# Kernel optimization log

Measured on AMD Instinct MI355X. Metric: run time of the kernel, lower is better.

Reference implementation:

```python
import jax, jax.numpy as jnp
import numpy as np

N = 768
C_IN = 128
C_OUT = 64
C_DGRAM = 39
C_AA = 22
C_ESM = 1280
LN_EPS = 1e-5


def _layer_norm(x, g, b):
    mu = jnp.mean(x, axis=-1, keepdims=True)
    var = jnp.var(x, axis=-1, keepdims=True)
    return (x - mu) * jax.lax.rsqrt(var + LN_EPS) * g + b


def setup_inputs() -> dict:
    key = jax.random.key(0)
    ks = jax.random.split(key, 36)
    rn = lambda k, s, sc=1.0: jax.random.normal(k, s, dtype=jnp.float32) * sc
    ru = lambda k, s: jax.random.uniform(k, s, dtype=jnp.float32)
    w = lambda k, cin: rn(k, (cin, C_OUT), 1.0 / np.sqrt(cin))
    z = jnp.zeros((C_OUT,), jnp.float32)
    return {
        "template_dgram": rn(ks[0], (N, N, C_DGRAM)),
        "aatype_one_hot": ru(ks[1], (N, C_AA)),
        "query_embedding": rn(ks[2], (N, N, C_IN)),
        "pseudo_beta_mask": ru(ks[3], (N,)),
        "backbone_mask": ru(ks[4], (N,)),
        "multichain_mask_2d": ru(ks[5], (N, N)),
        "unit_x": rn(ks[6], (N, N)),
        "unit_y": rn(ks[7], (N, N)),
        "unit_z": rn(ks[8], (N, N)),
        "esm_embedding": rn(ks[9], (N, C_ESM)),
        "w_dgram": w(ks[10], C_DGRAM), "b_dgram": z,
        "w_aa1": w(ks[11], C_AA), "b_aa1": z,
        "w_aa2": w(ks[12], C_AA), "b_aa2": z,
        "ln_g": jnp.ones((C_IN,), jnp.float32), "ln_b": jnp.zeros((C_IN,), jnp.float32),
        "w_q": w(ks[13], C_IN), "b_q": z,
        "w_pbm": w(ks[14], 1), "b_pbm": z,
        "w_x": w(ks[15], 1), "b_x": z,
        "w_y": w(ks[16], 1), "b_y": z,
        "w_z": w(ks[17], 1), "b_z": z,
        "w_bb": w(ks[18], 1), "b_bb": z,
        "w_esm1": w(ks[19], C_ESM), "b_esm1": z,
        "w_esm2": w(ks[20], C_ESM), "b_esm2": z,
    }


def reference(template_dgram, aatype_one_hot, query_embedding, pseudo_beta_mask,
              backbone_mask, multichain_mask_2d, unit_x, unit_y, unit_z, esm_embedding,
              w_dgram, b_dgram, w_aa1, b_aa1, w_aa2, b_aa2, ln_g, ln_b, w_q, b_q,
              w_pbm, b_pbm, w_x, b_x, w_y, b_y, w_z, b_z, w_bb, b_bb,
              w_esm1, b_esm1, w_esm2, b_esm2):
    # pair masks [N, N]
    pb2 = pseudo_beta_mask[:, None] * pseudo_beta_mask[None, :] * multichain_mask_2d
    bb2 = backbone_mask[:, None] * backbone_mask[None, :] * multichain_mask_2d
    # masked distogram -> GEMM over bins
    act = jnp.einsum('ijd,do->ijo', template_dgram * bb2[..., None], w_dgram) + b_dgram
    # Linear(1, c_out) branches: scalar * weight row + bias (broadcasts)
    act = act + (pb2[..., None] * w_pbm[0] + b_pbm)
    # per-residue aatype projections broadcast over rows / columns
    act = act + (aatype_one_hot @ w_aa1 + b_aa1)[None, :, :]
    act = act + (aatype_one_hot @ w_aa2 + b_aa2)[:, None, :]
    act = act + ((unit_x * bb2)[..., None] * w_x[0] + b_x)
    act = act + ((unit_y * bb2)[..., None] * w_y[0] + b_y)
    act = act + ((unit_z * bb2)[..., None] * w_z[0] + b_z)
    act = act + (bb2[..., None] * w_bb[0] + b_bb)
    # per-residue ESM projections broadcast over rows / columns
    act = act + (esm_embedding @ w_esm1 + b_esm1)[None, :, :]
    act = act + (esm_embedding @ w_esm2 + b_esm2)[:, None, :]
    # LayerNorm + projection of the query pair embedding [N, N, c_in]
    q = _layer_norm(query_embedding, ln_g, ln_b)
    act = act + jnp.einsum('ijc,co->ijo', q, w_q) + b_q
    return act
```

## Files before the change

### kernel.cpp

```cpp
#include <hip/hip_runtime.h>

#define NN 768
#define CIN 128
#define COUT 64
#define CDG 39
#define CAA 22
#define CESM 1280

typedef __attribute__((ext_vector_type(8))) short short8;
typedef __attribute__((ext_vector_type(4))) float f32x4;

__device__ __forceinline__ unsigned short f2bf(float f) {
  union { float f; unsigned int i; } c; c.f = f;
  unsigned int u = c.i;
  u += 0x7fffu + ((u >> 16) & 1u);
  return (unsigned short)(u >> 16);
}
__device__ __forceinline__ unsigned int pk(float a, float b) {
  return (unsigned int)f2bf(a) | ((unsigned int)f2bf(b) << 16);
}

struct Args {
  const float *td, *aa, *q, *pbm, *bbm, *mc, *ux, *uy, *uz, *esm;
  const float *w_dgram, *b_dgram, *w_aa1, *b_aa1, *w_aa2, *b_aa2;
  const float *ln_g, *ln_b, *w_q, *b_q;
  const float *w_pbm, *b_pbm, *w_x, *b_x, *w_y, *b_y, *w_z, *b_z, *w_bb, *b_bb;
  const float *w_esm1, *b_esm1, *w_esm2, *b_esm2;
  float* out;
  float* row_vec; float* col_vec; unsigned short* b_pack;
};

__global__ __launch_bounds__(256) void k_pre(Args a) {
  const int b = blockIdx.x;
  const int tid = threadIdx.x;
  if (b == NN) {
    for (int e = tid; e < 12288; e += 256) {
      int jj = e & 7;
      int lane = (e >> 3) & 63;
      int qt = e >> 9;
      int q = qt >> 2, t = qt & 3;
      int k = q * 32 + ((lane >> 4) << 3) + jj;
      int n = t * 16 + (lane & 15);
      float v = 0.f;
      if (k < CIN) v = a.w_q[k * COUT + n];
      else if (k < CIN + CDG) v = a.w_dgram[(k - CIN) * COUT + n];
      else if (k == 167) v = a.w_pbm[n];
      else if (k == 168) v = a.w_x[n];
      else if (k == 169) v = a.w_y[n];
      else if (k == 170) v = a.w_z[n];
      else if (k == 171) v = a.w_bb[n];
      a.b_pack[e] = f2bf(v);
    }
    return;
  }
  const int wv = tid >> 6, lane = tid & 63;
  float acc1 = 0.f, acc2 = 0.f;
  const int KT = CAA + CESM;
  const int SL = (KT + 3) / 4;
  int k0 = wv * SL;
  int k1 = k0 + SL; if (k1 > KT) k1 = KT;
  for (int k = k0; k < k1; ++k) {
    float v; const float *w1, *w2;
    if (k < CAA) { v = a.aa[b * CAA + k]; w1 = a.w_aa1 + k * COUT; w2 = a.w_aa2 + k * COUT; }
    else { int e = k - CAA; v = a.esm[b * CESM + e]; w1 = a.w_esm1 + e * COUT; w2 = a.w_esm2 + e * COUT; }
    acc1 += v * w1[lane];
    acc2 += v * w2[lane];
  }
  __shared__ float red1[4][64];
  __shared__ float red2[4][64];
  red1[wv][lane] = acc1; red2[wv][lane] = acc2;
  __syncthreads();
  if (wv == 0) {
    float r1 = red1[0][lane] + red1[1][lane] + red1[2][lane] + red1[3][lane];
    float r2 = red2[0][lane] + red2[1][lane] + red2[2][lane] + red2[3][lane];
    float br = a.b_aa1[lane] + a.b_esm1[lane] + a.b_dgram[lane] +
               a.b_pbm[lane] + a.b_x[lane] + a.b_y[lane] +
               a.b_z[lane] + a.b_bb[lane] + a.b_q[lane];
    float bc = a.b_aa2[lane] + a.b_esm2[lane];
    a.row_vec[b * COUT + lane] = r1 + br;
    a.col_vec[b * COUT + lane] = r2 + bc;
  }
}

__global__ __launch_bounds__(256, 3) void k_main(Args a) {
  const int jt = blockIdx.x;
  const int i  = blockIdx.y;
  const int jbase = jt * 64;
  const int tid = threadIdx.x;
  const int wv = tid >> 6, lane = tid & 63;

  __shared__ unsigned short A_lds[64][200];
  __shared__ unsigned short B_lds[12288];
  __shared__ float bb2_s[64];
  __shared__ float pb2_s[64];

  if (tid < 64) {
    int j = jbase + tid;
    float mc  = a.mc[(size_t)i * NN + j];
    bb2_s[tid] = a.bbm[i] * a.bbm[j] * mc;
    pb2_s[tid] = a.pbm[i] * a.pbm[j] * mc;
  }

  {
    const int4* src = (const int4*)a.b_pack;
    int4* dst = (int4*)B_lds;
#pragma unroll
    for (int r = 0; r < 6; ++r) dst[tid + 256 * r] = src[tid + 256 * r];
  }

  {
    const int p = tid >> 2, s = tid & 3;
    const float* qrow = a.q + ((size_t)i * NN + jbase + p) * CIN + s * 32;
    float q32[32];
    const float4* qv = (const float4*)qrow;
#pragma unroll
    for (int blk = 0; blk < 8; ++blk) {
      float4 t4 = qv[blk];
      q32[blk * 4 + 0] = t4.x; q32[blk * 4 + 1] = t4.y;
      q32[blk * 4 + 2] = t4.z; q32[blk * 4 + 3] = t4.w;
    }
    float sum = 0.f, sq = 0.f;
#pragma unroll
    for (int c = 0; c < 32; ++c) { sum += q32[c]; sq += q32[c] * q32[c]; }
    sum += __shfl_xor(sum, 1); sum += __shfl_xor(sum, 2);
    sq  += __shfl_xor(sq, 1);  sq  += __shfl_xor(sq, 2);
    float mu  = sum * (1.f / 128.f);
    float var = sq * (1.f / 128.f) - mu * mu;
    float rs  = rsqrtf(var + 1e-5f);
    float gl[32], bl[32];
    const float4* gv = (const float4*)(a.ln_g + s * 32);
    const float4* hv = (const float4*)(a.ln_b + s * 32);
#pragma unroll
    for (int blk = 0; blk < 8; ++blk) {
      float4 g4 = gv[blk], h4 = hv[blk];
      gl[blk * 4 + 0] = g4.x; gl[blk * 4 + 1] = g4.y;
      gl[blk * 4 + 2] = g4.z; gl[blk * 4 + 3] = g4.w;
      bl[blk * 4 + 0] = h4.x; bl[blk * 4 + 1] = h4.y;
      bl[blk * 4 + 2] = h4.z; bl[blk * 4 + 3] = h4.w;
    }
    int4* dA = (int4*)&A_lds[p][s * 32];
#pragma unroll
    for (int blk = 0; blk < 4; ++blk) {
      union { int4 v; unsigned int w[4]; } o;
#pragma unroll
      for (int w2 = 0; w2 < 4; ++w2) {
        int c = blk * 8 + w2 * 2;
        o.w[w2] = pk((q32[c] - mu) * rs * gl[c] + bl[c],
                     (q32[c + 1] - mu) * rs * gl[c + 1] + bl[c + 1]);
      }
      dA[blk] = o.v;
    }
  }
  __syncthreads();

  {
    const float* base = a.td + ((size_t)i * NN + jbase) * CDG;
    const float2* src = (const float2*)base;
    for (int w = tid; w < (64 * CDG) / 2; w += 256) {
      float2 d2 = src[w];
      int f0 = w * 2;
      int p0 = (f0 * 26887) >> 20; int d0 = f0 - p0 * CDG;
      int f1 = f0 + 1;
      int p1 = (f1 * 26887) >> 20; int d1 = f1 - p1 * CDG;
      A_lds[p0][CIN + d0] = f2bf(d2.x * bb2_s[p0]);
      A_lds[p1][CIN + d1] = f2bf(d2.y * bb2_s[p1]);
    }
  }
  if (tid < 64) {
    int p = tid;
    size_t gij = (size_t)i * NN + jbase + p;
    float bb = bb2_s[p];
    A_lds[p][167] = f2bf(pb2_s[p]);
    A_lds[p][168] = f2bf(a.ux[gij] * bb);
    A_lds[p][169] = f2bf(a.uy[gij] * bb);
    A_lds[p][170] = f2bf(a.uz[gij] * bb);
    A_lds[p][171] = f2bf(bb);
    unsigned int* zp = (unsigned int*)&A_lds[p][172];
#pragma unroll
    for (int z = 0; z < 10; ++z) zp[z] = 0;
  }
  __syncthreads();

  f32x4 acc[4];
#pragma unroll
  for (int t = 0; t < 4; ++t) { f32x4 z = {0.f, 0.f, 0.f, 0.f}; acc[t] = z; }
  const int m = lane & 15, quad = lane >> 4;
  const unsigned short* Ab = &A_lds[wv * 16 + m][quad * 8];
  const unsigned short* Bb = &B_lds[lane * 8];
#pragma unroll
  for (int q = 0; q < 6; ++q) {
    short8 af = *(const short8*)(Ab + q * 32);
#pragma unroll
    for (int t = 0; t < 4; ++t) {
      short8 bfr = *(const short8*)(Bb + (q * 4 + t) * 512);
      acc[t] = __builtin_amdgcn_mfma_f32_16x16x32_bf16(af, bfr, acc[t], 0, 0, 0);
    }
  }

  const float* cvp = a.col_vec + (size_t)i * COUT;
#pragma unroll
  for (int t = 0; t < 4; ++t) {
    int n = t * 16 + m;
    float cv = cvp[n];
#pragma unroll
    for (int r = 0; r < 4; ++r) {
      int p = wv * 16 + quad * 4 + r;
      int j = jbase + p;
      float val = acc[t][r] + a.row_vec[j * COUT + n] + cv;
      a.out[((size_t)i * NN + j) * COUT + n] = val;
    }
  }
}

extern "C" void kernel_launch(void* const* d_in, const int* in_sizes, int n_in,
                              void* d_out, int out_size, void* d_ws, size_t ws_size,
                              hipStream_t stream) {
  Args a;
  a.td     = (const float*)d_in[0];
  a.aa     = (const float*)d_in[1];
  a.q      = (const float*)d_in[2];
  a.pbm    = (const float*)d_in[3];
  a.bbm    = (const float*)d_in[4];
  a.mc     = (const float*)d_in[5];
  a.ux     = (const float*)d_in[6];
  a.uy     = (const float*)d_in[7];
  a.uz     = (const float*)d_in[8];
  a.esm    = (const float*)d_in[9];
  a.w_dgram = (const float*)d_in[10]; a.b_dgram = (const float*)d_in[11];
  a.w_aa1   = (const float*)d_in[12]; a.b_aa1   = (const float*)d_in[13];
  a.w_aa2   = (const float*)d_in[14]; a.b_aa2   = (const float*)d_in[15];
  a.ln_g    = (const float*)d_in[16]; a.ln_b    = (const float*)d_in[17];
  a.w_q     = (const float*)d_in[18]; a.b_q     = (const float*)d_in[19];
  a.w_pbm   = (const float*)d_in[20]; a.b_pbm   = (const float*)d_in[21];
  a.w_x     = (const float*)d_in[22]; a.b_x     = (const float*)d_in[23];
  a.w_y     = (const float*)d_in[24]; a.b_y     = (const float*)d_in[25];
  a.w_z     = (const float*)d_in[26]; a.b_z     = (const float*)d_in[27];
  a.w_bb    = (const float*)d_in[28]; a.b_bb    = (const float*)d_in[29];
  a.w_esm1  = (const float*)d_in[30]; a.b_esm1  = (const float*)d_in[31];
  a.w_esm2  = (const float*)d_in[32]; a.b_esm2  = (const float*)d_in[33];
  a.out = (float*)d_out;
  a.row_vec = (float*)d_ws;
  a.col_vec = a.row_vec + NN * COUT;
  a.b_pack  = (unsigned short*)(a.col_vec + NN * COUT);

  hipLaunchKernelGGL(k_pre, dim3(NN + 1), dim3(256), 0, stream, a);
  hipLaunchKernelGGL(k_main, dim3(12, NN), dim3(256), 0, stream, a);
}
```

Baseline: 803.5 us.

## Load query rows directly into MFMA fragments and fold LayerNorm affine into weights

Each lane now loads its query-embedding slice straight into registers in the MFMA A-fragment layout, computes the LayerNorm statistics with cross-lane shuffles, and packs bf16 fragments without staging them through LDS. The LayerNorm gain is folded into the packed w_q weights and the LayerNorm bias projection into the row bias vector in the pre-kernel. This shrinks the LDS A tile to the distogram and scalar part only and raises the occupancy hint from 3 to 4 blocks. The aim is to cut LDS traffic, LDS footprint and per-element arithmetic, at the cost of more live registers per thread.

```diff
diff --git a/kernel.cpp b/kernel.cpp
--- a/kernel.cpp
+++ b/kernel.cpp
@@ -42,7 +42,7 @@
       int k = q * 32 + ((lane >> 4) << 3) + jj;
       int n = t * 16 + (lane & 15);
       float v = 0.f;
-      if (k < CIN) v = a.w_q[k * COUT + n];
+      if (k < CIN) v = a.ln_g[k] * a.w_q[k * COUT + n];
       else if (k < CIN + CDG) v = a.w_dgram[(k - CIN) * COUT + n];
       else if (k == 167) v = a.w_pbm[n];
       else if (k == 168) v = a.w_x[n];
@@ -73,26 +73,37 @@
   if (wv == 0) {
     float r1 = red1[0][lane] + red1[1][lane] + red1[2][lane] + red1[3][lane];
     float r2 = red2[0][lane] + red2[1][lane] + red2[2][lane] + red2[3][lane];
+    float bq = 0.f;
+    for (int c = 0; c < CIN; ++c) bq += a.ln_b[c] * a.w_q[c * COUT + lane];
     float br = a.b_aa1[lane] + a.b_esm1[lane] + a.b_dgram[lane] +
                a.b_pbm[lane] + a.b_x[lane] + a.b_y[lane] +
-               a.b_z[lane] + a.b_bb[lane] + a.b_q[lane];
+               a.b_z[lane] + a.b_bb[lane] + a.b_q[lane] + bq;
     float bc = a.b_aa2[lane] + a.b_esm2[lane];
     a.row_vec[b * COUT + lane] = r1 + br;
     a.col_vec[b * COUT + lane] = r2 + bc;
   }
 }
 
-__global__ __launch_bounds__(256, 3) void k_main(Args a) {
+__global__ __launch_bounds__(256, 4) void k_main(Args a) {
   const int jt = blockIdx.x;
   const int i  = blockIdx.y;
   const int jbase = jt * 64;
   const int tid = threadIdx.x;
   const int wv = tid >> 6, lane = tid & 63;
-
-  __shared__ unsigned short A_lds[64][200];
+  const int m = lane & 15, quad = lane >> 4;
+
   __shared__ unsigned short B_lds[12288];
+  __shared__ unsigned short A2[64][72];
   __shared__ float bb2_s[64];
   __shared__ float pb2_s[64];
+
+  const float* qrow = a.q + ((size_t)i * NN + jbase + wv * 16 + m) * CIN + quad * 8;
+  float4 qv[8];
+#pragma unroll
+  for (int qq = 0; qq < 4; ++qq) {
+    qv[2 * qq]     = *(const float4*)(qrow + qq * 32);
+    qv[2 * qq + 1] = *(const float4*)(qrow + qq * 32 + 4);
+  }
 
   if (tid < 64) {
     int j = jbase + tid;
@@ -108,49 +119,31 @@
     for (int r = 0; r < 6; ++r) dst[tid + 256 * r] = src[tid + 256 * r];
   }
 
-  {
-    const int p = tid >> 2, s = tid & 3;
-    const float* qrow = a.q + ((size_t)i * NN + jbase + p) * CIN + s * 32;
-    float q32[32];
-    const float4* qv = (const float4*)qrow;
-#pragma unroll
-    for (int blk = 0; blk < 8; ++blk) {
-      float4 t4 = qv[blk];
-      q32[blk * 4 + 0] = t4.x; q32[blk * 4 + 1] = t4.y;
-      q32[blk * 4 + 2] = t4.z; q32[blk * 4 + 3] = t4.w;
-    }
-    float sum = 0.f, sq = 0.f;
-#pragma unroll
-    for (int c = 0; c < 32; ++c) { sum += q32[c]; sq += q32[c] * q32[c]; }
-    sum += __shfl_xor(sum, 1); sum += __shfl_xor(sum, 2);
-    sq  += __shfl_xor(sq, 1);  sq  += __shfl_xor(sq, 2);
-    float mu  = sum * (1.f / 128.f);
-    float var = sq * (1.f / 128.f) - mu * mu;
-    float rs  = rsqrtf(var + 1e-5f);
-    float gl[32], bl[32];
-    const float4* gv = (const float4*)(a.ln_g + s * 32);
-    const float4* hv = (const float4*)(a.ln_b + s * 32);
-#pragma unroll
-    for (int blk = 0; blk < 8; ++blk) {
-      float4 g4 = gv[blk], h4 = hv[blk];
-      gl[blk * 4 + 0] = g4.x; gl[blk * 4 + 1] = g4.y;
-      gl[blk * 4 + 2] = g4.z; gl[blk * 4 + 3] = g4.w;
-      bl[blk * 4 + 0] = h4.x; bl[blk * 4 + 1] = h4.y;
-      bl[blk * 4 + 2] = h4.z; bl[blk * 4 + 3] = h4.w;
-    }
-    int4* dA = (int4*)&A_lds[p][s * 32];
-#pragma unroll
-    for (int blk = 0; blk < 4; ++blk) {
-      union { int4 v; unsigned int w[4]; } o;
-#pragma unroll
-      for (int w2 = 0; w2 < 4; ++w2) {
-        int c = blk * 8 + w2 * 2;
-        o.w[w2] = pk((q32[c] - mu) * rs * gl[c] + bl[c],
-                     (q32[c + 1] - mu) * rs * gl[c + 1] + bl[c + 1]);
-      }
-      dA[blk] = o.v;
-    }
-  }
+  float sum = 0.f, sq = 0.f;
+#pragma unroll
+  for (int v = 0; v < 8; ++v) {
+    float4 t4 = qv[v];
+    sum += t4.x + t4.y + t4.z + t4.w;
+    sq  += t4.x * t4.x + t4.y * t4.y + t4.z * t4.z + t4.w * t4.w;
+  }
+  sum += __shfl_xor(sum, 16); sum += __shfl_xor(sum, 32);
+  sq  += __shfl_xor(sq, 16);  sq  += __shfl_xor(sq, 32);
+  const float mu  = sum * (1.f / 128.f);
+  const float var = sq * (1.f / 128.f) - mu * mu;
+  const float rs  = rsqrtf(var + 1e-5f);
+
+  short8 af[4];
+#pragma unroll
+  for (int qq = 0; qq < 4; ++qq) {
+    union { short8 s; unsigned int w[4]; } u;
+    float4 lo = qv[2 * qq], hi = qv[2 * qq + 1];
+    u.w[0] = pk((lo.x - mu) * rs, (lo.y - mu) * rs);
+    u.w[1] = pk((lo.z - mu) * rs, (lo.w - mu) * rs);
+    u.w[2] = pk((hi.x - mu) * rs, (hi.y - mu) * rs);
+    u.w[3] = pk((hi.z - mu) * rs, (hi.w - mu) * rs);
+    af[qq] = u.s;
+  }
+
   __syncthreads();
 
   {
@@ -162,20 +155,20 @@
       int p0 = (f0 * 26887) >> 20; int d0 = f0 - p0 * CDG;
       int f1 = f0 + 1;
       int p1 = (f1 * 26887) >> 20; int d1 = f1 - p1 * CDG;
-      A_lds[p0][CIN + d0] = f2bf(d2.x * bb2_s[p0]);
-      A_lds[p1][CIN + d1] = f2bf(d2.y * bb2_s[p1]);
+      A2[p0][d0] = f2bf(d2.x * bb2_s[p0]);
+      A2[p1][d1] = f2bf(d2.y * bb2_s[p1]);
     }
   }
   if (tid < 64) {
     int p = tid;
     size_t gij = (size_t)i * NN + jbase + p;
     float bb = bb2_s[p];
-    A_lds[p][167] = f2bf(pb2_s[p]);
-    A_lds[p][168] = f2bf(a.ux[gij] * bb);
-    A_lds[p][169] = f2bf(a.uy[gij] * bb);
-    A_lds[p][170] = f2bf(a.uz[gij] * bb);
-    A_lds[p][171] = f2bf(bb);
-    unsigned int* zp = (unsigned int*)&A_lds[p][172];
+    A2[p][39] = f2bf(pb2_s[p]);
+    A2[p][40] = f2bf(a.ux[gij] * bb);
+    A2[p][41] = f2bf(a.uy[gij] * bb);
+    A2[p][42] = f2bf(a.uz[gij] * bb);
+    A2[p][43] = f2bf(bb);
+    unsigned int* zp = (unsigned int*)&A2[p][44];
 #pragma unroll
     for (int z = 0; z < 10; ++z) zp[z] = 0;
   }
@@ -184,16 +177,23 @@
   f32x4 acc[4];
 #pragma unroll
   for (int t = 0; t < 4; ++t) { f32x4 z = {0.f, 0.f, 0.f, 0.f}; acc[t] = z; }
-  const int m = lane & 15, quad = lane >> 4;
-  const unsigned short* Ab = &A_lds[wv * 16 + m][quad * 8];
   const unsigned short* Bb = &B_lds[lane * 8];
 #pragma unroll
-  for (int q = 0; q < 6; ++q) {
-    short8 af = *(const short8*)(Ab + q * 32);
+  for (int qq = 0; qq < 4; ++qq) {
+#pragma unroll
+    for (int t = 0; t < 4; ++t) {
+      short8 bfr = *(const short8*)(Bb + (qq * 4 + t) * 512);
+      acc[t] = __builtin_amdgcn_mfma_f32_16x16x32_bf16(af[qq], bfr, acc[t], 0, 0, 0);
+    }
+  }
+  const unsigned short* Ab2 = &A2[wv * 16 + m][quad * 8];
+#pragma unroll
+  for (int q = 4; q < 6; ++q) {
+    short8 a8 = *(const short8*)(Ab2 + (q - 4) * 32);
 #pragma unroll
     for (int t = 0; t < 4; ++t) {
       short8 bfr = *(const short8*)(Bb + (q * 4 + t) * 512);
-      acc[t] = __builtin_amdgcn_mfma_f32_16x16x32_bf16(af, bfr, acc[t], 0, 0, 0);
+      acc[t] = __builtin_amdgcn_mfma_f32_16x16x32_bf16(a8, bfr, acc[t], 0, 0, 0);
     }
   }
 
```

Measured after the change: 744.5 us. -7.3%, faster.
